# Optimization experiments

Measured on AMD Instinct MI355X. Metric: run time of the kernel, lower is better.

The kernel has to match this reference:

```python
import jax, jax.numpy as jnp
import numpy as np

N, E, CIN, H, L = 50000, 800000, 128, 256, 3
EPS = 1e-5  # BatchNorm1d default eps


def setup_inputs() -> dict:
    key = jax.random.key(0)
    ks = jax.random.split(key, 24)
    x = jax.random.normal(ks[0], (N, CIN), dtype=jnp.float32)
    edge_index = jax.random.randint(ks[1], (2, E), 0, N, dtype=jnp.int64)
    params = {}
    cin = CIN
    for i in range(L):
        s = 1.0 / np.sqrt(cin).astype(np.float32)
        params[f"Wl{i}"] = jax.random.normal(ks[2 + 3 * i], (cin, H), dtype=jnp.float32) * s
        params[f"Wr{i}"] = jax.random.normal(ks[3 + 3 * i], (cin, H), dtype=jnp.float32) * s
        params[f"b{i}"] = jax.random.normal(ks[4 + 3 * i], (H,), dtype=jnp.float32) * 0.01
        cin = H
    gamma = jax.random.uniform(ks[20], (L, H), minval=0.5, maxval=1.5, dtype=jnp.float32)
    beta = jax.random.normal(ks[21], (L, H), dtype=jnp.float32) * 0.1
    rmean = jax.random.normal(ks[22], (L, H), dtype=jnp.float32) * 0.1
    rvar = jax.random.uniform(ks[23], (L, H), minval=0.5, maxval=1.5, dtype=jnp.float32)
    return dict(x=x, edge_index=edge_index, gamma=gamma, beta=beta,
                rmean=rmean, rvar=rvar, **params)


def reference(x, edge_index, gamma, beta, rmean, rvar,
              Wl0, Wr0, b0, Wl1, Wr1, b1, Wl2, Wr2, b2):
    src, dst = edge_index[0], edge_index[1]
    # in-degree of each destination node, clamped to 1 (mean aggregation)
    deg = jnp.maximum(
        jax.ops.segment_sum(jnp.ones((E,), jnp.float32), dst, num_segments=N), 1.0
    )[:, None]

    def layer(h, Wl, Wr, b, g, bt, rm, rv):
        # SAGEConv (mean): out = lin_l(mean_j x_j) + lin_r(x)
        agg = jax.ops.segment_sum(h[src], dst, num_segments=N) / deg  # [N, C]
        out = agg @ Wl + h @ Wr + b                                   # [N, H]
        # BatchNorm1d (eval mode: running stats) + ReLU; dropout is identity in eval
        out = (out - rm) * jax.lax.rsqrt(rv + EPS) * g + bt
        return jax.nn.relu(out)

    weights = [(Wl0, Wr0, b0), (Wl1, Wr1, b1), (Wl2, Wr2, b2)]
    for i, (Wl, Wr, b) in enumerate(weights):
        x = layer(x, Wl, Wr, b, gamma[i], beta[i], rmean[i], rvar[i])
    return x
```

## Files before the change

kernel.cpp:

```cpp
#include <hip/hip_runtime.h>
#include <hip/hip_bf16.h>

#define NN 50000
#define PADN 50048
#define EE 800000
#define HH 256
#define EPSBN 1e-5f
#define NBLK ((NN + 255) / 256)

typedef unsigned int uint32;
typedef __attribute__((ext_vector_type(8))) short short8;
typedef __attribute__((ext_vector_type(4))) float f32x4;
typedef __attribute__((ext_vector_type(2))) float f32x2;

__device__ __forceinline__ float bf2f(unsigned short u) {
    union { uint32 u; float f; } c; c.u = ((uint32)u) << 16; return c.f;
}
__device__ __forceinline__ unsigned short f2bf(float f) {
    __hip_bfloat16 h = __float2bfloat16(f);
    return *reinterpret_cast<unsigned short*>(&h);
}
__device__ __forceinline__ uint32 pkfp8(float a, float b, float c, float d) {
    int r = 0;
    r = __builtin_amdgcn_cvt_pk_fp8_f32(a, b, r, false);
    r = __builtin_amdgcn_cvt_pk_fp8_f32(c, d, r, true);
    return (uint32)r;
}


__global__ void count_rank(const int* __restrict__ dst, int* __restrict__ deg,
                           int* __restrict__ rank) {
    int e = blockIdx.x * blockDim.x + threadIdx.x;
    if (e < EE) rank[e] = atomicAdd(&deg[dst[e]], 1);
}

__global__ void scan_part(const int* __restrict__ deg, int* __restrict__ bsum) {
    __shared__ int sd[256];
    const int t = (int)threadIdx.x;
    const int i = (int)blockIdx.x * 256 + t;
    sd[t] = (i < NN) ? deg[i] : 0;
    __syncthreads();
    #pragma unroll
    for (int off = 128; off > 0; off >>= 1) {
        if (t < off) sd[t] += sd[t + off];
        __syncthreads();
    }
    if (t == 0) bsum[blockIdx.x] = sd[0];
}

__global__ void scan_top(const int* __restrict__ bsum, int* __restrict__ boff,
                         int* __restrict__ rowstart) {
    __shared__ int sd[256];
    const int t = (int)threadIdx.x;
    int v = (t < NBLK) ? bsum[t] : 0;
    sd[t] = v;
    __syncthreads();
    #pragma unroll
    for (int off = 1; off < 256; off <<= 1) {
        int u = (t >= off) ? sd[t - off] : 0;
        __syncthreads();
        sd[t] += u;
        __syncthreads();
    }
    if (t < NBLK) boff[t] = sd[t] - v;
    if (t == NBLK - 1) rowstart[NN] = sd[t];
}

__global__ void scan_fin(const int* __restrict__ deg, const int* __restrict__ boff,
                         int* __restrict__ rowstart) {
    __shared__ int sd[256];
    const int t = (int)threadIdx.x;
    const int i = (int)blockIdx.x * 256 + t;
    const int v = (i < NN) ? deg[i] : 0;
    sd[t] = v;
    __syncthreads();
    #pragma unroll
    for (int off = 1; off < 256; off <<= 1) {
        int u = (t >= off) ? sd[t - off] : 0;
        __syncthreads();
        sd[t] += u;
        __syncthreads();
    }
    if (i < NN) rowstart[i] = boff[blockIdx.x] + sd[t] - v;
}

__global__ void fill_csr2(const int* __restrict__ src, const int* __restrict__ dst,
                          const int* __restrict__ rank, const int* __restrict__ rowstart,
                          int* __restrict__ col) {
    int e = blockIdx.x * blockDim.x + threadIdx.x;
    if (e < EE) col[rowstart[dst[e]] + rank[e]] = src[e];
}


__global__ void cvt_x(const float* __restrict__ x, unsigned short* __restrict__ xb,
                      unsigned char* __restrict__ x8) {
    int i = blockIdx.x * blockDim.x + threadIdx.x;
    if (i >= PADN * 128 / 8) return;
    const int e0 = i * 8;
    float f[8];
    if (e0 + 8 <= NN * 128) {
        float4 u0 = *(const float4*)(x + e0);
        float4 u1 = *(const float4*)(x + e0 + 4);
        f[0] = u0.x; f[1] = u0.y; f[2] = u0.z; f[3] = u0.w;
        f[4] = u1.x; f[5] = u1.y; f[6] = u1.z; f[7] = u1.w;
    } else {
        #pragma unroll
        for (int k = 0; k < 8; ++k) f[k] = 0.f;
    }
    uint4 b;
    b.x = (uint32)f2bf(f[0]) | ((uint32)f2bf(f[1]) << 16);
    b.y = (uint32)f2bf(f[2]) | ((uint32)f2bf(f[3]) << 16);
    b.z = (uint32)f2bf(f[4]) | ((uint32)f2bf(f[5]) << 16);
    b.w = (uint32)f2bf(f[6]) | ((uint32)f2bf(f[7]) << 16);
    *(uint4*)(xb + e0) = b;
    uint2 p;
    p.x = pkfp8(f[0], f[1], f[2], f[3]);
    p.y = pkfp8(f[4], f[5], f[6], f[7]);
    *(uint2*)(x8 + e0) = p;
}

__global__ void pack_w(const float* __restrict__ Wl, const float* __restrict__ Wr,
                       unsigned short* __restrict__ Wpack, int C) {
    int idx = blockIdx.x * blockDim.x + threadIdx.x;
    if (idx >= 2 * C * 256) return;
    int e  = idx & 7;
    int l  = (idx >> 3) & 63;
    int nf = (idx >> 9) & 15;
    int s  = idx >> 13;
    int KS = C / 32;
    const float* W = (s < KS) ? Wl : Wr;
    int ks = (s < KS) ? s : s - KS;
    int k = ks * 32 + (l >> 4) * 8 + e;
    int n = nf * 16 + (l & 15);
    Wpack[idx] = f2bf(W[(size_t)k * HH + n]);
}


__device__ __forceinline__ void acc8f(float* a, uint2 v) {
    f32x2 f0 = __builtin_amdgcn_cvt_pk_f32_fp8(v.x, false);
    f32x2 f1 = __builtin_amdgcn_cvt_pk_f32_fp8(v.x, true);
    f32x2 f2 = __builtin_amdgcn_cvt_pk_f32_fp8(v.y, false);
    f32x2 f3 = __builtin_amdgcn_cvt_pk_f32_fp8(v.y, true);
    a[0] += f0.x; a[1] += f0.y; a[2] += f1.x; a[3] += f1.y;
    a[4] += f2.x; a[5] += f2.y; a[6] += f3.x; a[7] += f3.y;
}

template<int C>
__global__ void agg_mean_8(const unsigned char* __restrict__ h8, const int* __restrict__ rowstart,
                           const int* __restrict__ col,
                           unsigned short* __restrict__ agg) {
    const int wid = (int)((blockIdx.x * blockDim.x + threadIdx.x) >> 6);
    const int l   = (int)(threadIdx.x & 63);
    if (wid >= NN) return;
    const int beg = rowstart[wid], end = rowstart[wid + 1];
    const int d   = end - beg;
    const float inv = 1.0f / (float)(d > 1 ? d : 1);
    float a[8] = {0.f, 0.f, 0.f, 0.f, 0.f, 0.f, 0.f, 0.f};

    if (C == 256) {
        const int half = l >> 5;
        const int cl   = l & 31;
        const unsigned char* base = h8 + cl * 8;
        int j = beg + half;
        for (; j + 6 < end; j += 8) {
            int c0 = col[j], c1 = col[j + 2], c2 = col[j + 4], c3 = col[j + 6];
            uint2 v0 = *(const uint2*)(base + (size_t)c0 * C);
            uint2 v1 = *(const uint2*)(base + (size_t)c1 * C);
            uint2 v2 = *(const uint2*)(base + (size_t)c2 * C);
            uint2 v3 = *(const uint2*)(base + (size_t)c3 * C);
            acc8f(a, v0); acc8f(a, v1); acc8f(a, v2); acc8f(a, v3);
        }
        for (; j < end; j += 2) {
            uint2 v0 = *(const uint2*)(base + (size_t)col[j] * C);
            acc8f(a, v0);
        }
        #pragma unroll
        for (int k = 0; k < 8; ++k) a[k] += __shfl_xor(a[k], 32, 64);
        if (half == 0) {
            uint4 o;
            o.x = (uint32)f2bf(a[0] * inv) | ((uint32)f2bf(a[1] * inv) << 16);
            o.y = (uint32)f2bf(a[2] * inv) | ((uint32)f2bf(a[3] * inv) << 16);
            o.z = (uint32)f2bf(a[4] * inv) | ((uint32)f2bf(a[5] * inv) << 16);
            o.w = (uint32)f2bf(a[6] * inv) | ((uint32)f2bf(a[7] * inv) << 16);
            *(uint4*)(agg + (size_t)wid * C + cl * 8) = o;
        }
    } else {
        const int q  = l >> 4;
        const int cl = l & 15;
        const unsigned char* base = h8 + cl * 8;
        int j = beg + q;
        for (; j + 12 < end; j += 16) {
            int c0 = col[j], c1 = col[j + 4], c2 = col[j + 8], c3 = col[j + 12];
            uint2 v0 = *(const uint2*)(base + (size_t)c0 * C);
            uint2 v1 = *(const uint2*)(base + (size_t)c1 * C);
            uint2 v2 = *(const uint2*)(base + (size_t)c2 * C);
            uint2 v3 = *(const uint2*)(base + (size_t)c3 * C);
            acc8f(a, v0); acc8f(a, v1); acc8f(a, v2); acc8f(a, v3);
        }
        for (; j < end; j += 4) {
            uint2 v0 = *(const uint2*)(base + (size_t)col[j] * C);
            acc8f(a, v0);
        }
        #pragma unroll
        for (int k = 0; k < 8; ++k) {
            a[k] += __shfl_xor(a[k], 16, 64);
            a[k] += __shfl_xor(a[k], 32, 64);
        }
        if (q == 0) {
            uint4 o;
            o.x = (uint32)f2bf(a[0] * inv) | ((uint32)f2bf(a[1] * inv) << 16);
            o.y = (uint32)f2bf(a[2] * inv) | ((uint32)f2bf(a[3] * inv) << 16);
            o.z = (uint32)f2bf(a[4] * inv) | ((uint32)f2bf(a[5] * inv) << 16);
            o.w = (uint32)f2bf(a[6] * inv) | ((uint32)f2bf(a[7] * inv) << 16);
            *(uint4*)(agg + (size_t)wid * C + cl * 8) = o;
        }
    }
}


#define CPAD 260

template<int C, bool FINAL>
__global__ __launch_bounds__(256)
void gemm_mfma(const unsigned short* __restrict__ Aagg, const unsigned short* __restrict__ Ain,
               const unsigned short* __restrict__ Wpack,
               const float* __restrict__ bias, const float* __restrict__ gamma,
               const float* __restrict__ beta, const float* __restrict__ rmean,
               const float* __restrict__ rvar,
               float* __restrict__ outf, unsigned short* __restrict__ outb,
               unsigned char* __restrict__ out8)
{
    constexpr int KS = C / 32;
    constexpr int S  = 2 * KS;
    constexpr int NS = S / 2;
    __shared__ unsigned short Alds[2][4][1024];
    __shared__ __align__(16) unsigned char Cbuf[33280];
    const int tid = (int)threadIdx.x;
    const int wid = tid >> 6;
    const int l   = tid & 63;
    const int row0 = (int)blockIdx.x * 64;

    const int srow  = row0 + wid * 16 + (l & 15);
    const int skoff = (l >> 4) * 8;

    f32x4 acc[4][4];
    #pragma unroll
    for (int m = 0; m < 4; ++m)
        #pragma unroll
        for (int n = 0; n < 4; ++n)
            acc[m][n] = (f32x4){0.f, 0.f, 0.f, 0.f};

    auto stage = [&](int buf, int st) {
        #pragma unroll
        for (int k2 = 0; k2 < 2; ++k2) {
            const int s = st * 2 + k2;
            const unsigned short* Asrc = (s < KS) ? Aagg : Ain;
            const int ks = (s < KS) ? s : s - KS;
            const unsigned short* gp = Asrc + (size_t)srow * C + ks * 32 + skoff;
            __builtin_amdgcn_global_load_lds(
                (const __attribute__((address_space(1))) uint32*)gp,
                (__attribute__((address_space(3))) uint32*)(&Alds[buf][wid][k2 * 512]),
                16, 0, 0);
        }
    };

    stage(0, 0);
    int cur = 0;
    for (int st = 0; st < NS; ++st) {
        __syncthreads();
        if (st + 1 < NS) stage(cur ^ 1, st + 1);
        short8 b[2][4];
        #pragma unroll
        for (int k2 = 0; k2 < 2; ++k2)
            #pragma unroll
            for (int n = 0; n < 4; ++n) {
                size_t off = ((size_t)(st * 2 + k2) * 16 + wid * 4 + n) * 512 + l * 8;
                b[k2][n] = *(const short8*)(Wpack + off);
            }
        short8 a[2][4];
        #pragma unroll
        for (int k2 = 0; k2 < 2; ++k2)
            #pragma unroll
            for (int m = 0; m < 4; ++m)
                a[k2][m] = *(const short8*)(&Alds[cur][m][k2 * 512 + l * 8]);
        #pragma unroll
        for (int k2 = 0; k2 < 2; ++k2)
            #pragma unroll
            for (int m = 0; m < 4; ++m)
                #pragma unroll
                for (int n = 0; n < 4; ++n)
                    acc[m][n] = __builtin_amdgcn_mfma_f32_16x16x32_bf16(a[k2][m], b[k2][n], acc[m][n], 0, 0, 0);
        cur ^= 1;
    }

    float sj[4], cj[4];
    #pragma unroll
    for (int n = 0; n < 4; ++n) {
        const int jj = wid * 64 + n * 16 + (l & 15);
        sj[n] = gamma[jj] * rsqrtf(rvar[jj] + EPSBN);
        cj[n] = (bias[jj] - rmean[jj]) * sj[n] + beta[jj];
    }

    if (FINAL) {
        float* Cf = (float*)Cbuf;
        #pragma unroll
        for (int half = 0; half < 2; ++half) {
            if (half) __syncthreads();
            #pragma unroll
            for (int n = 0; n < 4; ++n) {
                const int jj = wid * 64 + n * 16 + (l & 15);
                #pragma unroll
                for (int mm = 0; mm < 2; ++mm) {
                    const int m  = half * 2 + mm;
                    const int rb = mm * 16 + (l >> 4) * 4;
                    #pragma unroll
                    for (int j = 0; j < 4; ++j) {
                        float v = acc[m][n][j] * sj[n] + cj[n];
                        Cf[(rb + j) * CPAD + jj] = v > 0.f ? v : 0.f;
                    }
                }
            }
            __syncthreads();
            const int col4 = (tid & 63) * 4;
            const int rw   = tid >> 6;
            #pragma unroll
            for (int i = 0; i < 8; ++i) {
                const int row  = i * 4 + rw;
                const int grow = row0 + half * 32 + row;
                if (grow < NN) {
                    float4 v = *(const float4*)&Cf[row * CPAD + col4];
                    *(float4*)(outf + (size_t)grow * HH + col4) = v;
                }
            }
        }
    } else {
        unsigned short* Clds = (unsigned short*)Cbuf;
        #pragma unroll
        for (int n = 0; n < 4; ++n) {
            const int jj = wid * 64 + n * 16 + (l & 15);
            #pragma unroll
            for (int m = 0; m < 4; ++m) {
                const int rb = m * 16 + (l >> 4) * 4;
                #pragma unroll
                for (int j = 0; j < 4; ++j) {
                    float v = acc[m][n][j] * sj[n] + cj[n];
                    Clds[(rb + j) * CPAD + jj] = f2bf(v > 0.f ? v : 0.f);
                }
            }
        }
        __syncthreads();
        #pragma unroll
        for (int i = 0; i < 8; ++i) {
            const int row  = i * 8 + (tid >> 5);
            const int col8 = (tid & 31) * 8;
            uint4 v = *(const uint4*)&Clds[row * CPAD + col8];
            *(uint4*)(outb + ((size_t)(row0 + row)) * HH + col8) = v;
            uint2 p;
            p.x = pkfp8(bf2f((unsigned short)(v.x & 0xffff)), bf2f((unsigned short)(v.x >> 16)),
                        bf2f((unsigned short)(v.y & 0xffff)), bf2f((unsigned short)(v.y >> 16)));
            p.y = pkfp8(bf2f((unsigned short)(v.z & 0xffff)), bf2f((unsigned short)(v.z >> 16)),
                        bf2f((unsigned short)(v.w & 0xffff)), bf2f((unsigned short)(v.w >> 16)));
            *(uint2*)(out8 + ((size_t)(row0 + row)) * HH + col8) = p;
        }
    }
}


static inline size_t alignup(size_t x) { return (x + 511) & ~(size_t)511; }

extern "C" void kernel_launch(void* const* d_in, const int* in_sizes, int n_in,
                              void* d_out, int out_size, void* d_ws, size_t ws_size,
                              hipStream_t stream) {
    const float* x   = (const float*)d_in[0];
    const int*   ei  = (const int*)d_in[1];
    const int*   src = ei;
    const int*   dst = ei + EE;
    const float* gamma = (const float*)d_in[2];
    const float* beta  = (const float*)d_in[3];
    const float* rmean = (const float*)d_in[4];
    const float* rvar  = (const float*)d_in[5];
    const float* Wl0 = (const float*)d_in[6];
    const float* Wr0 = (const float*)d_in[7];
    const float* b0  = (const float*)d_in[8];
    const float* Wl1 = (const float*)d_in[9];
    const float* Wr1 = (const float*)d_in[10];
    const float* b1  = (const float*)d_in[11];
    const float* Wl2 = (const float*)d_in[12];
    const float* Wr2 = (const float*)d_in[13];
    const float* b2  = (const float*)d_in[14];
    float* out = (float*)d_out;
    (void)ws_size; (void)n_in; (void)in_sizes; (void)out_size;

    char* w = (char*)d_ws;
    size_t off = 0;
    int*   deg      = (int*)(w + off);   off += alignup(NN * 4);
    int*   rank     = (int*)(w + off);   off += alignup((size_t)EE * 4);
    int*   rowstart = (int*)(w + off);   off += alignup((NN + 1) * 4);
    int*   bsum     = (int*)(w + off);   off += alignup(NBLK * 4);
    int*   boff     = (int*)(w + off);   off += alignup(NBLK * 4);
    int*   col      = (int*)(w + off);   off += alignup((size_t)EE * 4);
    unsigned short* xb   = (unsigned short*)(w + off); off += alignup((size_t)PADN * 128 * 2);
    unsigned short* agg  = (unsigned short*)(w + off); off += alignup((size_t)PADN * HH * 2);
    unsigned short* h1   = (unsigned short*)(w + off); off += alignup((size_t)PADN * HH * 2);
    unsigned short* h2   = (unsigned short*)(w + off); off += alignup((size_t)PADN * HH * 2);
    unsigned char*  x8   = (unsigned char*)(w + off);  off += alignup((size_t)PADN * 128);
    unsigned char*  h1_8 = (unsigned char*)(w + off);  off += alignup((size_t)PADN * HH);
    unsigned char*  h2_8 = (unsigned char*)(w + off);  off += alignup((size_t)PADN * HH);
    unsigned short* Wp0  = (unsigned short*)(w + off); off += alignup((size_t)2 * 128 * 256 * 2);
    unsigned short* Wp1  = (unsigned short*)(w + off); off += alignup((size_t)2 * 256 * 256 * 2);
    unsigned short* Wp2  = (unsigned short*)(w + off); off += alignup((size_t)2 * 256 * 256 * 2);

    hipMemsetAsync(deg, 0, NN * 4, stream);
    count_rank<<<(EE + 255) / 256, 256, 0, stream>>>(dst, deg, rank);
    scan_part<<<NBLK, 256, 0, stream>>>(deg, bsum);
    scan_top <<<1, 256, 0, stream>>>(bsum, boff, rowstart);
    scan_fin <<<NBLK, 256, 0, stream>>>(deg, boff, rowstart);
    fill_csr2<<<(EE + 255) / 256, 256, 0, stream>>>(src, dst, rank, rowstart, col);

    cvt_x <<<(PADN * 128 / 8 + 255) / 256, 256, 0, stream>>>(x, xb, x8);
    pack_w<<<(2 * 128 * 256 + 255) / 256, 256, 0, stream>>>(Wl0, Wr0, Wp0, 128);
    pack_w<<<(2 * 256 * 256 + 255) / 256, 256, 0, stream>>>(Wl1, Wr1, Wp1, 256);
    pack_w<<<(2 * 256 * 256 + 255) / 256, 256, 0, stream>>>(Wl2, Wr2, Wp2, 256);

    const int agg_grid  = (NN * 64 + 255) / 256;
    const int gemm_grid = PADN / 64;

    agg_mean_8<128><<<agg_grid, 256, 0, stream>>>(x8, rowstart, col, agg);
    gemm_mfma<128, false><<<gemm_grid, 256, 0, stream>>>(agg, xb, Wp0,
        b0, gamma + 0 * HH, beta + 0 * HH, rmean + 0 * HH, rvar + 0 * HH, nullptr, h1, h1_8);

    agg_mean_8<256><<<agg_grid, 256, 0, stream>>>(h1_8, rowstart, col, agg);
    gemm_mfma<256, false><<<gemm_grid, 256, 0, stream>>>(agg, h1, Wp1,
        b1, gamma + 1 * HH, beta + 1 * HH, rmean + 1 * HH, rvar + 1 * HH, nullptr, h2, h2_8);

    agg_mean_8<256><<<agg_grid, 256, 0, stream>>>(h2_8, rowstart, col, agg);
    gemm_mfma<256, true><<<gemm_grid, 256, 0, stream>>>(agg, h2, Wp2,
        b2, gamma + 2 * HH, beta + 2 * HH, rmean + 2 * HH, rvar + 2 * HH, out, nullptr, nullptr);
}
```

Measured before the change: 340.3 us.

## Fuse neighbor aggregation into the GEMM kernel and trim preprocessing launches

Each layer now runs one kernel. A block first gathers and mean-aggregates the fp8 neighbor features for its 64 rows straight into a swizzled shared-memory tile, then runs the MFMA GEMM against that tile and the staged self-features. This removes the intermediate agg buffer round-trip through global memory and one launch per layer. Preprocessing is also compacted: the deg memset is folded into cvt_x, the three-pass scan becomes two kernels, and the three weight-pack launches become one. The trade-off is lower gather parallelism per block (one wave handles 16 rows serially), more LDS per block, and the launch bound of 3 may limit registers.

```diff
diff --git a/kernel.cpp b/kernel.cpp
--- a/kernel.cpp
+++ b/kernel.cpp
@@ -28,73 +28,10 @@
 }
 
 
-__global__ void count_rank(const int* __restrict__ dst, int* __restrict__ deg,
-                           int* __restrict__ rank) {
-    int e = blockIdx.x * blockDim.x + threadIdx.x;
-    if (e < EE) rank[e] = atomicAdd(&deg[dst[e]], 1);
-}
-
-__global__ void scan_part(const int* __restrict__ deg, int* __restrict__ bsum) {
-    __shared__ int sd[256];
-    const int t = (int)threadIdx.x;
-    const int i = (int)blockIdx.x * 256 + t;
-    sd[t] = (i < NN) ? deg[i] : 0;
-    __syncthreads();
-    #pragma unroll
-    for (int off = 128; off > 0; off >>= 1) {
-        if (t < off) sd[t] += sd[t + off];
-        __syncthreads();
-    }
-    if (t == 0) bsum[blockIdx.x] = sd[0];
-}
-
-__global__ void scan_top(const int* __restrict__ bsum, int* __restrict__ boff,
-                         int* __restrict__ rowstart) {
-    __shared__ int sd[256];
-    const int t = (int)threadIdx.x;
-    int v = (t < NBLK) ? bsum[t] : 0;
-    sd[t] = v;
-    __syncthreads();
-    #pragma unroll
-    for (int off = 1; off < 256; off <<= 1) {
-        int u = (t >= off) ? sd[t - off] : 0;
-        __syncthreads();
-        sd[t] += u;
-        __syncthreads();
-    }
-    if (t < NBLK) boff[t] = sd[t] - v;
-    if (t == NBLK - 1) rowstart[NN] = sd[t];
-}
-
-__global__ void scan_fin(const int* __restrict__ deg, const int* __restrict__ boff,
-                         int* __restrict__ rowstart) {
-    __shared__ int sd[256];
-    const int t = (int)threadIdx.x;
-    const int i = (int)blockIdx.x * 256 + t;
-    const int v = (i < NN) ? deg[i] : 0;
-    sd[t] = v;
-    __syncthreads();
-    #pragma unroll
-    for (int off = 1; off < 256; off <<= 1) {
-        int u = (t >= off) ? sd[t - off] : 0;
-        __syncthreads();
-        sd[t] += u;
-        __syncthreads();
-    }
-    if (i < NN) rowstart[i] = boff[blockIdx.x] + sd[t] - v;
-}
-
-__global__ void fill_csr2(const int* __restrict__ src, const int* __restrict__ dst,
-                          const int* __restrict__ rank, const int* __restrict__ rowstart,
-                          int* __restrict__ col) {
-    int e = blockIdx.x * blockDim.x + threadIdx.x;
-    if (e < EE) col[rowstart[dst[e]] + rank[e]] = src[e];
-}
-
-
 __global__ void cvt_x(const float* __restrict__ x, unsigned short* __restrict__ xb,
-                      unsigned char* __restrict__ x8) {
+                      unsigned char* __restrict__ x8, int* __restrict__ deg) {
     int i = blockIdx.x * blockDim.x + threadIdx.x;
+    if (i < NN) deg[i] = 0;
     if (i >= PADN * 128 / 8) return;
     const int e0 = i * 8;
     float f[8];
@@ -119,20 +56,88 @@
     *(uint2*)(x8 + e0) = p;
 }
 
-__global__ void pack_w(const float* __restrict__ Wl, const float* __restrict__ Wr,
-                       unsigned short* __restrict__ Wpack, int C) {
-    int idx = blockIdx.x * blockDim.x + threadIdx.x;
-    if (idx >= 2 * C * 256) return;
+__global__ void count_rank(const int* __restrict__ dst, int* __restrict__ deg,
+                           int* __restrict__ rank) {
+    int e = blockIdx.x * blockDim.x + threadIdx.x;
+    if (e < EE) rank[e] = atomicAdd(&deg[dst[e]], 1);
+}
+
+__global__ void scan_part(const int* __restrict__ deg, int* __restrict__ bsum) {
+    __shared__ int sd[256];
+    const int t = (int)threadIdx.x;
+    const int i = (int)blockIdx.x * 256 + t;
+    sd[t] = (i < NN) ? deg[i] : 0;
+    __syncthreads();
+    #pragma unroll
+    for (int off = 128; off > 0; off >>= 1) {
+        if (t < off) sd[t] += sd[t + off];
+        __syncthreads();
+    }
+    if (t == 0) bsum[blockIdx.x] = sd[0];
+}
+
+__global__ void scan_fin(const int* __restrict__ deg, const int* __restrict__ bsum,
+                         int* __restrict__ rowstart) {
+    __shared__ int sb[256];
+    __shared__ int sd[256];
+    const int t = (int)threadIdx.x;
+    const int b = (int)blockIdx.x;
+    sb[t] = (t < NBLK && t < b) ? bsum[t] : 0;
+    __syncthreads();
+    #pragma unroll
+    for (int off = 128; off > 0; off >>= 1) {
+        if (t < off) sb[t] += sb[t + off];
+        __syncthreads();
+    }
+    const int boff = sb[0];
+    const int i = b * 256 + t;
+    const int v = (i < NN) ? deg[i] : 0;
+    sd[t] = v;
+    __syncthreads();
+    #pragma unroll
+    for (int off = 1; off < 256; off <<= 1) {
+        int u = (t >= off) ? sd[t - off] : 0;
+        __syncthreads();
+        sd[t] += u;
+        __syncthreads();
+    }
+    if (i < NN) rowstart[i] = boff + sd[t] - v;
+    if (i == 0) rowstart[NN] = EE;
+}
+
+__global__ void fill_csr2(const int* __restrict__ src, const int* __restrict__ dst,
+                          const int* __restrict__ rank, const int* __restrict__ rowstart,
+                          int* __restrict__ col) {
+    int e = blockIdx.x * blockDim.x + threadIdx.x;
+    if (e < EE) col[rowstart[dst[e]] + rank[e]] = src[e];
+}
+
+__device__ __forceinline__ void pack_one(const float* __restrict__ Wl,
+                                         const float* __restrict__ Wr,
+                                         unsigned short* __restrict__ Wp,
+                                         int C, int idx) {
     int e  = idx & 7;
-    int l  = (idx >> 3) & 63;
+    int ll = (idx >> 3) & 63;
     int nf = (idx >> 9) & 15;
     int s  = idx >> 13;
-    int KS = C / 32;
-    const float* W = (s < KS) ? Wl : Wr;
-    int ks = (s < KS) ? s : s - KS;
-    int k = ks * 32 + (l >> 4) * 8 + e;
-    int n = nf * 16 + (l & 15);
-    Wpack[idx] = f2bf(W[(size_t)k * HH + n]);
+    int KSl = C / 32;
+    const float* W = (s < KSl) ? Wl : Wr;
+    int ks = (s < KSl) ? s : s - KSl;
+    int k = ks * 32 + (ll >> 4) * 8 + e;
+    int n = nf * 16 + (ll & 15);
+    Wp[idx] = f2bf(W[(size_t)k * HH + n]);
+}
+
+__global__ void pack_w3(const float* __restrict__ Wl0, const float* __restrict__ Wr0,
+                        unsigned short* __restrict__ Wp0,
+                        const float* __restrict__ Wl1, const float* __restrict__ Wr1,
+                        unsigned short* __restrict__ Wp1,
+                        const float* __restrict__ Wl2, const float* __restrict__ Wr2,
+                        unsigned short* __restrict__ Wp2) {
+    int idx = blockIdx.x * blockDim.x + threadIdx.x;
+    if (idx < 65536)       pack_one(Wl0, Wr0, Wp0, 128, idx);
+    else if (idx < 196608) pack_one(Wl1, Wr1, Wp1, 256, idx - 65536);
+    else if (idx < 327680) pack_one(Wl2, Wr2, Wp2, 256, idx - 196608);
 }
 
 
@@ -145,144 +150,148 @@
     a[4] += f2.x; a[5] += f2.y; a[6] += f3.x; a[7] += f3.y;
 }
 
-template<int C>
-__global__ void agg_mean_8(const unsigned char* __restrict__ h8, const int* __restrict__ rowstart,
-                           const int* __restrict__ col,
-                           unsigned short* __restrict__ agg) {
-    const int wid = (int)((blockIdx.x * blockDim.x + threadIdx.x) >> 6);
-    const int l   = (int)(threadIdx.x & 63);
-    if (wid >= NN) return;
-    const int beg = rowstart[wid], end = rowstart[wid + 1];
-    const int d   = end - beg;
-    const float inv = 1.0f / (float)(d > 1 ? d : 1);
-    float a[8] = {0.f, 0.f, 0.f, 0.f, 0.f, 0.f, 0.f, 0.f};
-
-    if (C == 256) {
-        const int half = l >> 5;
-        const int cl   = l & 31;
-        const unsigned char* base = h8 + cl * 8;
-        int j = beg + half;
-        for (; j + 6 < end; j += 8) {
-            int c0 = col[j], c1 = col[j + 2], c2 = col[j + 4], c3 = col[j + 6];
-            uint2 v0 = *(const uint2*)(base + (size_t)c0 * C);
-            uint2 v1 = *(const uint2*)(base + (size_t)c1 * C);
-            uint2 v2 = *(const uint2*)(base + (size_t)c2 * C);
-            uint2 v3 = *(const uint2*)(base + (size_t)c3 * C);
-            acc8f(a, v0); acc8f(a, v1); acc8f(a, v2); acc8f(a, v3);
-        }
-        for (; j < end; j += 2) {
-            uint2 v0 = *(const uint2*)(base + (size_t)col[j] * C);
-            acc8f(a, v0);
-        }
-        #pragma unroll
-        for (int k = 0; k < 8; ++k) a[k] += __shfl_xor(a[k], 32, 64);
-        if (half == 0) {
-            uint4 o;
-            o.x = (uint32)f2bf(a[0] * inv) | ((uint32)f2bf(a[1] * inv) << 16);
-            o.y = (uint32)f2bf(a[2] * inv) | ((uint32)f2bf(a[3] * inv) << 16);
-            o.z = (uint32)f2bf(a[4] * inv) | ((uint32)f2bf(a[5] * inv) << 16);
-            o.w = (uint32)f2bf(a[6] * inv) | ((uint32)f2bf(a[7] * inv) << 16);
-            *(uint4*)(agg + (size_t)wid * C + cl * 8) = o;
-        }
-    } else {
-        const int q  = l >> 4;
-        const int cl = l & 15;
-        const unsigned char* base = h8 + cl * 8;
-        int j = beg + q;
-        for (; j + 12 < end; j += 16) {
-            int c0 = col[j], c1 = col[j + 4], c2 = col[j + 8], c3 = col[j + 12];
-            uint2 v0 = *(const uint2*)(base + (size_t)c0 * C);
-            uint2 v1 = *(const uint2*)(base + (size_t)c1 * C);
-            uint2 v2 = *(const uint2*)(base + (size_t)c2 * C);
-            uint2 v3 = *(const uint2*)(base + (size_t)c3 * C);
-            acc8f(a, v0); acc8f(a, v1); acc8f(a, v2); acc8f(a, v3);
-        }
-        for (; j < end; j += 4) {
-            uint2 v0 = *(const uint2*)(base + (size_t)col[j] * C);
-            acc8f(a, v0);
-        }
-        #pragma unroll
-        for (int k = 0; k < 8; ++k) {
-            a[k] += __shfl_xor(a[k], 16, 64);
-            a[k] += __shfl_xor(a[k], 32, 64);
-        }
-        if (q == 0) {
-            uint4 o;
-            o.x = (uint32)f2bf(a[0] * inv) | ((uint32)f2bf(a[1] * inv) << 16);
-            o.y = (uint32)f2bf(a[2] * inv) | ((uint32)f2bf(a[3] * inv) << 16);
-            o.z = (uint32)f2bf(a[4] * inv) | ((uint32)f2bf(a[5] * inv) << 16);
-            o.w = (uint32)f2bf(a[6] * inv) | ((uint32)f2bf(a[7] * inv) << 16);
-            *(uint4*)(agg + (size_t)wid * C + cl * 8) = o;
-        }
-    }
-}
-
-
 #define CPAD 260
 
 template<int C, bool FINAL>
-__global__ __launch_bounds__(256)
-void gemm_mfma(const unsigned short* __restrict__ Aagg, const unsigned short* __restrict__ Ain,
-               const unsigned short* __restrict__ Wpack,
-               const float* __restrict__ bias, const float* __restrict__ gamma,
-               const float* __restrict__ beta, const float* __restrict__ rmean,
-               const float* __restrict__ rvar,
-               float* __restrict__ outf, unsigned short* __restrict__ outb,
-               unsigned char* __restrict__ out8)
+__global__ __launch_bounds__(256, 3)
+void layer_fused(const unsigned char* __restrict__ g8,
+                 const unsigned short* __restrict__ hb,
+                 const int* __restrict__ rowstart, const int* __restrict__ colx,
+                 const unsigned short* __restrict__ Wpack,
+                 const float* __restrict__ bias, const float* __restrict__ gamma,
+                 const float* __restrict__ beta, const float* __restrict__ rmean,
+                 const float* __restrict__ rvar,
+                 float* __restrict__ outf, unsigned short* __restrict__ outb,
+                 unsigned char* __restrict__ out8)
 {
     constexpr int KS = C / 32;
-    constexpr int S  = 2 * KS;
-    constexpr int NS = S / 2;
+    constexpr int NH = KS / 2;
     __shared__ unsigned short Alds[2][4][1024];
     __shared__ __align__(16) unsigned char Cbuf[33280];
     const int tid = (int)threadIdx.x;
     const int wid = tid >> 6;
     const int l   = tid & 63;
     const int row0 = (int)blockIdx.x * 64;
-
-    const int srow  = row0 + wid * 16 + (l & 15);
-    const int skoff = (l >> 4) * 8;
-
-    f32x4 acc[4][4];
-    #pragma unroll
-    for (int m = 0; m < 4; ++m)
-        #pragma unroll
-        for (int n = 0; n < 4; ++n)
-            acc[m][n] = (f32x4){0.f, 0.f, 0.f, 0.f};
-
-    auto stage = [&](int buf, int st) {
+    const int srow = row0 + wid * 16 + (l & 15);
+    const int skb  = (l >> 4) * 16;
+
+    auto stage_h = [&](int buf, int hs) {
         #pragma unroll
         for (int k2 = 0; k2 < 2; ++k2) {
-            const int s = st * 2 + k2;
-            const unsigned short* Asrc = (s < KS) ? Aagg : Ain;
-            const int ks = (s < KS) ? s : s - KS;
-            const unsigned short* gp = Asrc + (size_t)srow * C + ks * 32 + skoff;
+            const int kh = hs * 2 + k2;
+            const unsigned short* gp = hb + (size_t)srow * C + kh * 32 + (l >> 4) * 8;
             __builtin_amdgcn_global_load_lds(
                 (const __attribute__((address_space(1))) uint32*)gp,
                 (__attribute__((address_space(3))) uint32*)(&Alds[buf][wid][k2 * 512]),
                 16, 0, 0);
         }
     };
-
-    stage(0, 0);
-    int cur = 0;
-    for (int st = 0; st < NS; ++st) {
-        __syncthreads();
-        if (st + 1 < NS) stage(cur ^ 1, st + 1);
-        short8 b[2][4];
-        #pragma unroll
-        for (int k2 = 0; k2 < 2; ++k2)
-            #pragma unroll
-            for (int n = 0; n < 4; ++n) {
-                size_t off = ((size_t)(st * 2 + k2) * 16 + wid * 4 + n) * 512 + l * 8;
-                b[k2][n] = *(const short8*)(Wpack + off);
-            }
-        short8 a[2][4];
-        #pragma unroll
-        for (int k2 = 0; k2 < 2; ++k2)
-            #pragma unroll
-            for (int m = 0; m < 4; ++m)
-                a[k2][m] = *(const short8*)(&Alds[cur][m][k2 * 512 + l * 8]);
+    stage_h(0, 0);
+    if (NH > 1) stage_h(1, 1);
+
+    if (C == 256) {
+        const int half = l >> 5, cl = l & 31;
+        const unsigned char* base = g8 + cl * 8;
+        for (int i = 0; i < 16; ++i) {
+            const int nd = row0 + wid * 16 + i;
+            float a[8] = {0.f, 0.f, 0.f, 0.f, 0.f, 0.f, 0.f, 0.f};
+            float inv = 1.f;
+            if (nd < NN) {
+                const int beg = rowstart[nd], end = rowstart[nd + 1];
+                const int d = end - beg;
+                inv = 1.0f / (float)(d > 1 ? d : 1);
+                int j = beg + half;
+                for (; j + 6 < end; j += 8) {
+                    int c0 = colx[j], c1 = colx[j + 2], c2 = colx[j + 4], c3 = colx[j + 6];
+                    uint2 v0 = *(const uint2*)(base + (size_t)c0 * C);
+                    uint2 v1 = *(const uint2*)(base + (size_t)c1 * C);
+                    uint2 v2 = *(const uint2*)(base + (size_t)c2 * C);
+                    uint2 v3 = *(const uint2*)(base + (size_t)c3 * C);
+                    acc8f(a, v0); acc8f(a, v1); acc8f(a, v2); acc8f(a, v3);
+                }
+                for (; j < end; j += 2) {
+                    uint2 v0 = *(const uint2*)(base + (size_t)colx[j] * C);
+                    acc8f(a, v0);
+                }
+            }
+            #pragma unroll
+            for (int k = 0; k < 8; ++k) a[k] += __shfl_xor(a[k], 32, 64);
+            if (half == 0) {
+                const int r = wid * 16 + i;
+                uint4 o;
+                o.x = (uint32)f2bf(a[0] * inv) | ((uint32)f2bf(a[1] * inv) << 16);
+                o.y = (uint32)f2bf(a[2] * inv) | ((uint32)f2bf(a[3] * inv) << 16);
+                o.z = (uint32)f2bf(a[4] * inv) | ((uint32)f2bf(a[5] * inv) << 16);
+                o.w = (uint32)f2bf(a[6] * inv) | ((uint32)f2bf(a[7] * inv) << 16);
+                *(uint4*)(Cbuf + r * 512 + ((cl * 16) ^ ((r & 7) << 4))) = o;
+            }
+        }
+    } else {
+        const int q = l >> 4, cl = l & 15;
+        const unsigned char* base = g8 + cl * 8;
+        for (int i = 0; i < 16; ++i) {
+            const int nd = row0 + wid * 16 + i;
+            float a[8] = {0.f, 0.f, 0.f, 0.f, 0.f, 0.f, 0.f, 0.f};
+            float inv = 1.f;
+            if (nd < NN) {
+                const int beg = rowstart[nd], end = rowstart[nd + 1];
+                const int d = end - beg;
+                inv = 1.0f / (float)(d > 1 ? d : 1);
+                int j = beg + q;
+                for (; j + 12 < end; j += 16) {
+                    int c0 = colx[j], c1 = colx[j + 4], c2 = colx[j + 8], c3 = colx[j + 12];
+                    uint2 v0 = *(const uint2*)(base + (size_t)c0 * C);
+                    uint2 v1 = *(const uint2*)(base + (size_t)c1 * C);
+                    uint2 v2 = *(const uint2*)(base + (size_t)c2 * C);
+                    uint2 v3 = *(const uint2*)(base + (size_t)c3 * C);
+                    acc8f(a, v0); acc8f(a, v1); acc8f(a, v2); acc8f(a, v3);
+                }
+                for (; j < end; j += 4) {
+                    uint2 v0 = *(const uint2*)(base + (size_t)colx[j] * C);
+                    acc8f(a, v0);
+                }
+            }
+            #pragma unroll
+            for (int k = 0; k < 8; ++k) {
+                a[k] += __shfl_xor(a[k], 16, 64);
+                a[k] += __shfl_xor(a[k], 32, 64);
+            }
+            if (q == 0) {
+                const int r = wid * 16 + i;
+                uint4 o;
+                o.x = (uint32)f2bf(a[0] * inv) | ((uint32)f2bf(a[1] * inv) << 16);
+                o.y = (uint32)f2bf(a[2] * inv) | ((uint32)f2bf(a[3] * inv) << 16);
+                o.z = (uint32)f2bf(a[4] * inv) | ((uint32)f2bf(a[5] * inv) << 16);
+                o.w = (uint32)f2bf(a[6] * inv) | ((uint32)f2bf(a[7] * inv) << 16);
+                *(uint4*)(Cbuf + r * 256 + ((cl * 16) ^ ((r & 7) << 4))) = o;
+            }
+        }
+    }
+    __syncthreads();
+
+    f32x4 acc[4][4];
+    #pragma unroll
+    for (int m = 0; m < 4; ++m)
+        #pragma unroll
+        for (int n = 0; n < 4; ++n)
+            acc[m][n] = (f32x4){0.f, 0.f, 0.f, 0.f};
+
+    #pragma unroll
+    for (int st = 0; st < KS / 2; ++st) {
+        short8 b[2][4], a[2][4];
+        #pragma unroll
+        for (int k2 = 0; k2 < 2; ++k2)
+            #pragma unroll
+            for (int n = 0; n < 4; ++n)
+                b[k2][n] = *(const short8*)(Wpack + ((size_t)(st * 2 + k2) * 16 + wid * 4 + n) * 512 + l * 8);
+        #pragma unroll
+        for (int k2 = 0; k2 < 2; ++k2)
+            #pragma unroll
+            for (int m = 0; m < 4; ++m) {
+                const int row = m * 16 + (l & 15);
+                const int ks  = st * 2 + k2;
+                a[k2][m] = *(const short8*)(Cbuf + row * (2 * C) + ((ks * 64 + skb) ^ ((row & 7) << 4)));
+            }
         #pragma unroll
         for (int k2 = 0; k2 < 2; ++k2)
             #pragma unroll
@@ -290,7 +299,31 @@
                 #pragma unroll
                 for (int n = 0; n < 4; ++n)
                     acc[m][n] = __builtin_amdgcn_mfma_f32_16x16x32_bf16(a[k2][m], b[k2][n], acc[m][n], 0, 0, 0);
-        cur ^= 1;
+    }
+    #pragma unroll
+    for (int hs = 0; hs < NH; ++hs) {
+        __syncthreads();
+        if (hs >= 1 && hs + 1 < NH) stage_h((hs + 1) & 1, hs + 1);
+        short8 b[2][4], a[2][4];
+        #pragma unroll
+        for (int k2 = 0; k2 < 2; ++k2)
+            #pragma unroll
+            for (int n = 0; n < 4; ++n) {
+                const int s = KS + hs * 2 + k2;
+                b[k2][n] = *(const short8*)(Wpack + ((size_t)s * 16 + wid * 4 + n) * 512 + l * 8);
+            }
+        #pragma unroll
+        for (int k2 = 0; k2 < 2; ++k2)
+            #pragma unroll
+            for (int m = 0; m < 4; ++m)
+                a[k2][m] = *(const short8*)(&Alds[hs & 1][m][k2 * 512 + l * 8]);
+        #pragma unroll
+        for (int k2 = 0; k2 < 2; ++k2)
+            #pragma unroll
+            for (int m = 0; m < 4; ++m)
+                #pragma unroll
+                for (int n = 0; n < 4; ++n)
+                    acc[m][n] = __builtin_amdgcn_mfma_f32_16x16x32_bf16(a[k2][m], b[k2][n], acc[m][n], 0, 0, 0);
     }
 
     float sj[4], cj[4];
@@ -305,7 +338,7 @@
         float* Cf = (float*)Cbuf;
         #pragma unroll
         for (int half = 0; half < 2; ++half) {
-            if (half) __syncthreads();
+            __syncthreads();
             #pragma unroll
             for (int n = 0; n < 4; ++n) {
                 const int jj = wid * 64 + n * 16 + (l & 15);
@@ -335,6 +368,7 @@
         }
     } else {
         unsigned short* Clds = (unsigned short*)Cbuf;
+        __syncthreads();
         #pragma unroll
         for (int n = 0; n < 4; ++n) {
             const int jj = wid * 64 + n * 16 + (l & 15);
@@ -397,10 +431,8 @@
     int*   rank     = (int*)(w + off);   off += alignup((size_t)EE * 4);
     int*   rowstart = (int*)(w + off);   off += alignup((NN + 1) * 4);
     int*   bsum     = (int*)(w + off);   off += alignup(NBLK * 4);
-    int*   boff     = (int*)(w + off);   off += alignup(NBLK * 4);
     int*   col      = (int*)(w + off);   off += alignup((size_t)EE * 4);
     unsigned short* xb   = (unsigned short*)(w + off); off += alignup((size_t)PADN * 128 * 2);
-    unsigned short* agg  = (unsigned short*)(w + off); off += alignup((size_t)PADN * HH * 2);
     unsigned short* h1   = (unsigned short*)(w + off); off += alignup((size_t)PADN * HH * 2);
     unsigned short* h2   = (unsigned short*)(w + off); off += alignup((size_t)PADN * HH * 2);
     unsigned char*  x8   = (unsigned char*)(w + off);  off += alignup((size_t)PADN * 128);
@@ -410,30 +442,21 @@
     unsigned short* Wp1  = (unsigned short*)(w + off); off += alignup((size_t)2 * 256 * 256 * 2);
     unsigned short* Wp2  = (unsigned short*)(w + off); off += alignup((size_t)2 * 256 * 256 * 2);
 
-    hipMemsetAsync(deg, 0, NN * 4, stream);
+    cvt_x     <<<(PADN * 128 / 8 + 255) / 256, 256, 0, stream>>>(x, xb, x8, deg);
     count_rank<<<(EE + 255) / 256, 256, 0, stream>>>(dst, deg, rank);
-    scan_part<<<NBLK, 256, 0, stream>>>(deg, bsum);
-    scan_top <<<1, 256, 0, stream>>>(bsum, boff, rowstart);
-    scan_fin <<<NBLK, 256, 0, stream>>>(deg, boff, rowstart);
-    fill_csr2<<<(EE + 255) / 256, 256, 0, stream>>>(src, dst, rank, rowstart, col);
-
-    cvt_x <<<(PADN * 128 / 8 + 255) / 256, 256, 0, stream>>>(x, xb, x8);
-    pack_w<<<(2 * 128 * 256 + 255) / 256, 256, 0, stream>>>(Wl0, Wr0, Wp0, 128);
-    pack_w<<<(2 * 256 * 256 + 255) / 256, 256, 0, stream>>>(Wl1, Wr1, Wp1, 256);
-    pack_w<<<(2 * 256 * 256 + 255) / 256, 256, 0, stream>>>(Wl2, Wr2, Wp2, 256);
-
-    const int agg_grid  = (NN * 64 + 255) / 256;
-    const int gemm_grid = PADN / 64;
-
-    agg_mean_8<128><<<agg_grid, 256, 0, stream>>>(x8, rowstart, col, agg);
-    gemm_mfma<128, false><<<gemm_grid, 256, 0, stream>>>(agg, xb, Wp0,
+    scan_part <<<NBLK, 256, 0, stream>>>(deg, bsum);
+    scan_fin  <<<NBLK, 256, 0, stream>>>(deg, bsum, rowstart);
+    fill_csr2 <<<(EE + 255) / 256, 256, 0, stream>>>(src, dst, rank, rowstart, col);
+    pack_w3   <<<1280, 256, 0, stream>>>(Wl0, Wr0, Wp0, Wl1, Wr1, Wp1, Wl2, Wr2, Wp2);
+
+    const int lgrid = PADN / 64;
+
+    layer_fused<128, false><<<lgrid, 256, 0, stream>>>(x8, xb, rowstart, col, Wp0,
         b0, gamma + 0 * HH, beta + 0 * HH, rmean + 0 * HH, rvar + 0 * HH, nullptr, h1, h1_8);
 
-    agg_mean_8<256><<<agg_grid, 256, 0, stream>>>(h1_8, rowstart, col, agg);
-    gemm_mfma<256, false><<<gemm_grid, 256, 0, stream>>>(agg, h1, Wp1,
+    layer_fused<256, false><<<lgrid, 256, 0, stream>>>(h1_8, h1, rowstart, col, Wp1,
         b1, gamma + 1 * HH, beta + 1 * HH, rmean + 1 * HH, rvar + 1 * HH, nullptr, h2, h2_8);
 
-    agg_mean_8<256><<<agg_grid, 256, 0, stream>>>(h2_8, rowstart, col, agg);
-    gemm_mfma<256, true><<<gemm_grid, 256, 0, stream>>>(agg, h2, Wp2,
+    layer_fused<256, true><<<lgrid, 256, 0, stream>>>(h2_8, h2, rowstart, col, Wp2,
         b2, gamma + 2 * HH, beta + 2 * HH, rmean + 2 * HH, rvar + 2 * HH, out, nullptr, nullptr);
 }
```

Measured after the change: 475.4 us. 39.7% more time.
